# Optimization experiments

Hardware: AMD Instinct MI355X
Metric: run time of the kernel (lower is better)

Reference implementation:

```python
import jax, jax.numpy as jnp
import numpy as np

B, S, D_MODEL, D_K, D_V = 4, 2048, 1024, 64, 64


def setup_inputs() -> dict:
    key = jax.random.key(0)
    ks = jax.random.split(key, 6)
    Q = jax.random.normal(ks[0], (B, S, D_MODEL), dtype=jnp.float32)
    K = jax.random.normal(ks[1], (B, S, D_MODEL), dtype=jnp.float32)
    V = jax.random.normal(ks[2], (B, S, D_MODEL), dtype=jnp.float32)
    # Linear weights stored as [in, out] so projection is x @ W
    scale = 1.0 / np.sqrt(D_MODEL)
    WQ = jax.random.normal(ks[3], (D_MODEL, D_K), dtype=jnp.float32) * scale
    WK = jax.random.normal(ks[4], (D_MODEL, D_K), dtype=jnp.float32) * scale
    WV = jax.random.normal(ks[5], (D_MODEL, D_V), dtype=jnp.float32) * scale
    # causal mask: 1 = attend, 0 = masked (torch masked_fill(mask == 0, -inf))
    mask = jnp.tril(jnp.ones((S, S), dtype=jnp.int32))
    return {"Q": Q, "K": K, "V": V, "WQ": WQ, "WK": WK, "WV": WV, "mask": mask}


def reference(Q, K, V, WQ, WK, WV, mask):
    d_k = WQ.shape[-1]
    q = jnp.einsum("bsd,dk->bsk", Q, WQ)   # [B,S,d_k]
    k = jnp.einsum("bsd,dk->bsk", K, WK)   # [B,S,d_k]
    v = jnp.einsum("bsd,dv->bsv", V, WV)   # [B,S,d_v]
    scores = jnp.einsum("bqk,bsk->bqs", q, k) / jnp.sqrt(jnp.float32(d_k))
    scores = jnp.where(mask == 0, -jnp.inf, scores)  # broadcast [S,S] over batch
    attn = jax.nn.softmax(scores, axis=-1)
    H = jnp.einsum("bqs,bsv->bqv", attn, v)  # [B,S,d_v]
    return H
```

## Files before the change

### kernel.cpp

```cpp
#include <hip/hip_runtime.h>

typedef unsigned int u32;
typedef unsigned short u16;
using bf16x8 = __attribute__((ext_vector_type(8))) short;
using f32x4  = __attribute__((ext_vector_type(4))) float;

#define MFMA16 __builtin_amdgcn_mfma_f32_16x16x32_bf16

#define QH  (0u)
#define QL  (1u<<20)
#define KHO (2u<<20)
#define KLO (3u<<20)
#define VHO (4u<<20)
#define VLO (5u<<20)
#define VTH (6u<<20)
#define VTL (7u<<20)
#define WTH (8u<<20)
#define WTL (WTH + 3u*64*1024*2)
#define OPOFF (9u<<20)
#define PMOFF (OPOFF + 576u*4096*4)
#define PLOFF (PMOFF + 576u*64*4)

__device__ __forceinline__ u16 f2bf(float x) {
    u32 u = __float_as_uint(x);
    return (u16)((u + 0x7FFFu + ((u >> 16) & 1u)) >> 16);
}
__device__ __forceinline__ float bf2f(u16 h) {
    return __uint_as_float(((u32)h) << 16);
}

__device__ __forceinline__ int swz(int row, int c) {
    return c ^ ((row ^ (row >> 3)) & 7);
}
__device__ __forceinline__ bf16x8 ldsf(const char* t, int row, int c) {
    return *reinterpret_cast<const bf16x8*>(t + row * 128 + swz(row, c) * 16);
}
__device__ __forceinline__ void ldst(char* t, int row, int c, bf16x8 v) {
    *reinterpret_cast<bf16x8*>(t + row * 128 + swz(row, c) * 16) = v;
}

__device__ __forceinline__ void stage_bf16(char* tile, const u16* g, int ldu, int t) {
    const int row = t >> 2, cg = t & 3;
    const char* gp = reinterpret_cast<const char*>(g + (size_t)row * ldu + cg * 16);
    bf16x8 a = *reinterpret_cast<const bf16x8*>(gp);
    bf16x8 b = *reinterpret_cast<const bf16x8*>(gp + 16);
    ldst(tile, row, cg * 2, a);
    ldst(tile, row, cg * 2 + 1, b);
}

__device__ __forceinline__ void stage_split(char* th, char* tl, const float* g, int ld, int t) {
    const int row = t >> 2, cg = t & 3;
    const float* gp = g + (size_t)row * ld + cg * 16;
    #pragma unroll
    for (int c = 0; c < 2; ++c) {
        bf16x8 h, l;
        #pragma unroll
        for (int j = 0; j < 8; ++j) {
            float x = gp[c * 8 + j];
            u16 hb = f2bf(x);
            u16 lb = f2bf(x - bf2f(hb));
            h[j] = (short)hb; l[j] = (short)lb;
        }
        ldst(th, row, cg * 2 + c, h);
        ldst(tl, row, cg * 2 + c, l);
    }
}

__global__ __launch_bounds__(256) void wsplit_kernel(const float* __restrict__ WQ,
                                                     const float* __restrict__ WK,
                                                     const float* __restrict__ WV,
                                                     char* __restrict__ ws) {
    const int p = blockIdx.y, kt = blockIdx.x;
    const float* W = (p == 0) ? WQ : (p == 1) ? WK : WV;
    __shared__ float lds[64 * 68];
    const int t = threadIdx.x, row = t >> 2, cg = t & 3;
    const float* gp = W + ((size_t)kt * 64 + row) * 64 + cg * 16;
    #pragma unroll
    for (int j = 0; j < 16; ++j) lds[row * 68 + cg * 16 + j] = gp[j];
    __syncthreads();
    const int n = row, d0 = cg * 16;
    u32 wh[8], wl[8];
    #pragma unroll
    for (int j = 0; j < 8; ++j) {
        float x0 = lds[(d0 + 2 * j) * 68 + n];
        float x1 = lds[(d0 + 2 * j + 1) * 68 + n];
        u16 h0 = f2bf(x0), h1 = f2bf(x1);
        u16 l0 = f2bf(x0 - bf2f(h0)), l1 = f2bf(x1 - bf2f(h1));
        wh[j] = (u32)h0 | ((u32)h1 << 16);
        wl[j] = (u32)l0 | ((u32)l1 << 16);
    }
    u16* oh = (u16*)(ws + WTH) + (size_t)p * 64 * 1024 + (size_t)n * 1024 + kt * 64 + d0;
    u16* ol = (u16*)(ws + WTL) + (size_t)p * 64 * 1024 + (size_t)n * 1024 + kt * 64 + d0;
    uint4 a = {wh[0], wh[1], wh[2], wh[3]}, b = {wh[4], wh[5], wh[6], wh[7]};
    uint4 c = {wl[0], wl[1], wl[2], wl[3]}, d = {wl[4], wl[5], wl[6], wl[7]};
    *reinterpret_cast<uint4*>(oh) = a; *reinterpret_cast<uint4*>(oh + 8) = b;
    *reinterpret_cast<uint4*>(ol) = c; *reinterpret_cast<uint4*>(ol + 8) = d;
}

__global__ __launch_bounds__(256) void proj_kernel(const float* __restrict__ Q,
                                                   const float* __restrict__ K,
                                                   const float* __restrict__ V,
                                                   char* __restrict__ ws) {
    const int p = blockIdx.y;
    const float* X = (p == 0) ? Q : (p == 1) ? K : V;
    const u16* wth = (const u16*)(ws + WTH) + (size_t)p * 64 * 1024;
    const u16* wtl = (const u16*)(ws + WTL) + (size_t)p * 64 * 1024;
    u16* oh = (u16*)(ws + ((p == 0) ? QH : (p == 1) ? KHO : VHO));
    u16* ol = (u16*)(ws + ((p == 0) ? QL : (p == 1) ? KLO : VLO));
    const int rt = blockIdx.x;
    __shared__ char xh[8192], xl[8192], bh_[8192], bl_[8192];
    const int t = threadIdx.x, lane = t & 63, w = t >> 6;
    f32x4 acc[4];
    #pragma unroll
    for (int nt = 0; nt < 4; ++nt) acc[nt] = (f32x4){0.f, 0.f, 0.f, 0.f};
    for (int kc = 0; kc < 1024; kc += 64) {
        __syncthreads();
        stage_split(xh, xl, X + (size_t)rt * 64 * 1024 + kc, 1024, t);
        stage_bf16(bh_, wth + kc, 1024, t);
        stage_bf16(bl_, wtl + kc, 1024, t);
        __syncthreads();
        #pragma unroll
        for (int s = 0; s < 2; ++s) {
            bf16x8 ah = ldsf(xh, w * 16 + (lane & 15), s * 4 + (lane >> 4));
            bf16x8 al = ldsf(xl, w * 16 + (lane & 15), s * 4 + (lane >> 4));
            #pragma unroll
            for (int nt = 0; nt < 4; ++nt) {
                bf16x8 bh = ldsf(bh_, nt * 16 + (lane & 15), s * 4 + (lane >> 4));
                bf16x8 bl = ldsf(bl_, nt * 16 + (lane & 15), s * 4 + (lane >> 4));
                acc[nt] = MFMA16(ah, bh, acc[nt], 0, 0, 0);
                acc[nt] = MFMA16(ah, bl, acc[nt], 0, 0, 0);
                acc[nt] = MFMA16(al, bh, acc[nt], 0, 0, 0);
            }
        }
    }
    const float qs = (p == 0) ? 0.125f : 1.0f;
    #pragma unroll
    for (int nt = 0; nt < 4; ++nt)
        #pragma unroll
        for (int r = 0; r < 4; ++r) {
            float v = acc[nt][r] * qs;
            u16 hb = f2bf(v);
            u16 lb = f2bf(v - bf2f(hb));
            size_t idx = ((size_t)rt * 64 + w * 16 + (lane >> 4) * 4 + r) * 64 + nt * 16 + (lane & 15);
            oh[idx] = hb; ol[idx] = lb;
        }
}

__global__ __launch_bounds__(256) void vt_kernel(char* __restrict__ ws) {
    const int st = blockIdx.x, b = blockIdx.y;
    __shared__ u16 lh[64 * 72], ll[64 * 72];
    const int t = threadIdx.x, row = t >> 2, cg = t & 3;
    const u16* vh = (const u16*)(ws + VHO) + ((size_t)b * 2048 + st * 64 + row) * 64 + cg * 16;
    const u16* vl = (const u16*)(ws + VLO) + ((size_t)b * 2048 + st * 64 + row) * 64 + cg * 16;
    *reinterpret_cast<uint4*>(&lh[row * 72 + cg * 16]) = *reinterpret_cast<const uint4*>(vh);
    *reinterpret_cast<uint4*>(&lh[row * 72 + cg * 16 + 8]) = *reinterpret_cast<const uint4*>(vh + 8);
    *reinterpret_cast<uint4*>(&ll[row * 72 + cg * 16]) = *reinterpret_cast<const uint4*>(vl);
    *reinterpret_cast<uint4*>(&ll[row * 72 + cg * 16 + 8]) = *reinterpret_cast<const uint4*>(vl + 8);
    __syncthreads();
    const int d = row, s0 = cg * 16;
    u32 wh[8], wl[8];
    #pragma unroll
    for (int j = 0; j < 8; ++j) {
        wh[j] = (u32)lh[(s0 + 2 * j) * 72 + d] | ((u32)lh[(s0 + 2 * j + 1) * 72 + d] << 16);
        wl[j] = (u32)ll[(s0 + 2 * j) * 72 + d] | ((u32)ll[(s0 + 2 * j + 1) * 72 + d] << 16);
    }
    u16* th = (u16*)(ws + VTH) + ((size_t)b * 64 + d) * 2048 + st * 64 + s0;
    u16* tl = (u16*)(ws + VTL) + ((size_t)b * 64 + d) * 2048 + st * 64 + s0;
    uint4 a = {wh[0], wh[1], wh[2], wh[3]}, bb = {wh[4], wh[5], wh[6], wh[7]};
    uint4 c = {wl[0], wl[1], wl[2], wl[3]}, dd = {wl[4], wl[5], wl[6], wl[7]};
    *reinterpret_cast<uint4*>(th) = a; *reinterpret_cast<uint4*>(th + 8) = bb;
    *reinterpret_cast<uint4*>(tl) = c; *reinterpret_cast<uint4*>(tl + 8) = dd;
}

__device__ __forceinline__ int slot_base(int qt) {
    const int q4 = qt >> 2, r = qt & 3;
    return qt + 2 * q4 * (q4 - 1) + r * q4;
}

__global__ __launch_bounds__(256) void attn_kernel(char* __restrict__ ws) {
    const int chunk = blockIdx.x;
    const int qt = 31 - blockIdx.y;
    const int b = blockIdx.z;
    const int Li = qt + 1, kt0 = chunk * 4;
    if (kt0 >= Li) return;
    const int kt1 = (kt0 + 4 < Li) ? kt0 + 4 : Li;
    __shared__ char kh[8192], kl[8192], vh[8192], vl[8192], ph[8192], pl[8192];
    const int t = threadIdx.x, lane = t & 63, w = t >> 6;
    const u16* qhg = (const u16*)(ws + QH);
    const u16* qlg = (const u16*)(ws + QL);
    const size_t qrow = (size_t)b * 2048 + qt * 64 + w * 16 + (lane & 15);
    bf16x8 qfh[2], qfl[2];
    #pragma unroll
    for (int s = 0; s < 2; ++s) {
        qfh[s] = *reinterpret_cast<const bf16x8*>(qhg + qrow * 64 + s * 32 + (lane >> 4) * 8);
        qfl[s] = *reinterpret_cast<const bf16x8*>(qlg + qrow * 64 + s * 32 + (lane >> 4) * 8);
    }
    const u16* kgh = (const u16*)(ws + KHO) + (size_t)b * 2048 * 64;
    const u16* kgl = (const u16*)(ws + KLO) + (size_t)b * 2048 * 64;
    const u16* vgh = (const u16*)(ws + VTH) + (size_t)b * 64 * 2048;
    const u16* vgl = (const u16*)(ws + VTL) + (size_t)b * 64 * 2048;
    f32x4 o[4];
    #pragma unroll
    for (int nt = 0; nt < 4; ++nt) o[nt] = (f32x4){0.f, 0.f, 0.f, 0.f};
    float mrow[4], lrow[4];
    #pragma unroll
    for (int r = 0; r < 4; ++r) { mrow[r] = -1e30f; lrow[r] = 0.f; }
    for (int kt = kt0; kt < kt1; ++kt) {
        __syncthreads();
        stage_bf16(kh, kgh + (size_t)kt * 64 * 64, 64, t);
        stage_bf16(kl, kgl + (size_t)kt * 64 * 64, 64, t);
        stage_bf16(vh, vgh + kt * 64, 2048, t);
        stage_bf16(vl, vgl + kt * 64, 2048, t);
        __syncthreads();
        f32x4 sacc[4];
        #pragma unroll
        for (int nt = 0; nt < 4; ++nt) sacc[nt] = (f32x4){0.f, 0.f, 0.f, 0.f};
        #pragma unroll
        for (int s = 0; s < 2; ++s) {
            #pragma unroll
            for (int nt = 0; nt < 4; ++nt) {
                bf16x8 bh = ldsf(kh, nt * 16 + (lane & 15), s * 4 + (lane >> 4));
                bf16x8 bl = ldsf(kl, nt * 16 + (lane & 15), s * 4 + (lane >> 4));
                sacc[nt] = MFMA16(qfh[s], bh, sacc[nt], 0, 0, 0);
                sacc[nt] = MFMA16(qfh[s], bl, sacc[nt], 0, 0, 0);
                sacc[nt] = MFMA16(qfl[s], bh, sacc[nt], 0, 0, 0);
            }
        }
        if (kt == qt) {
            #pragma unroll
            for (int nt = 0; nt < 4; ++nt)
                #pragma unroll
                for (int r = 0; r < 4; ++r)
                    if (nt * 16 + (lane & 15) > w * 16 + (lane >> 4) * 4 + r)
                        sacc[nt][r] = -1e30f;
        }
        float pcur[4][4], scv[4];
        #pragma unroll
        for (int r = 0; r < 4; ++r) {
            float mx = fmaxf(fmaxf(sacc[0][r], sacc[1][r]), fmaxf(sacc[2][r], sacc[3][r]));
            #pragma unroll
            for (int off = 1; off < 16; off <<= 1) mx = fmaxf(mx, __shfl_xor(mx, off));
            const float nm = fmaxf(mrow[r], mx);
            scv[r] = __expf(mrow[r] - nm);
            mrow[r] = nm;
            float rs = 0.f;
            #pragma unroll
            for (int nt = 0; nt < 4; ++nt) {
                float pv = __expf(sacc[nt][r] - nm);
                pcur[nt][r] = pv; rs += pv;
            }
            #pragma unroll
            for (int off = 1; off < 16; off <<= 1) rs += __shfl_xor(rs, off);
            lrow[r] = lrow[r] * scv[r] + rs;
        }
        f32x4 scq = {scv[0], scv[1], scv[2], scv[3]};
        #pragma unroll
        for (int nt = 0; nt < 4; ++nt) o[nt] *= scq;
        #pragma unroll
        for (int nt = 0; nt < 4; ++nt)
            #pragma unroll
            for (int r = 0; r < 4; ++r) {
                const int row = w * 16 + (lane >> 4) * 4 + r;
                const int key = nt * 16 + (lane & 15);
                u16 hb = f2bf(pcur[nt][r]);
                u16 lb = f2bf(pcur[nt][r] - bf2f(hb));
                const int byt = row * 128 + swz(row, key >> 3) * 16 + (key & 7) * 2;
                *reinterpret_cast<u16*>(ph + byt) = hb;
                *reinterpret_cast<u16*>(pl + byt) = lb;
            }
        #pragma unroll
        for (int s = 0; s < 2; ++s) {
            bf16x8 pah = ldsf(ph, w * 16 + (lane & 15), s * 4 + (lane >> 4));
            bf16x8 pal = ldsf(pl, w * 16 + (lane & 15), s * 4 + (lane >> 4));
            #pragma unroll
            for (int nt = 0; nt < 4; ++nt) {
                bf16x8 vbh = ldsf(vh, nt * 16 + (lane & 15), s * 4 + (lane >> 4));
                bf16x8 vbl = ldsf(vl, nt * 16 + (lane & 15), s * 4 + (lane >> 4));
                o[nt] = MFMA16(pah, vbh, o[nt], 0, 0, 0);
                o[nt] = MFMA16(pah, vbl, o[nt], 0, 0, 0);
                o[nt] = MFMA16(pal, vbh, o[nt], 0, 0, 0);
            }
        }
    }
    const int slot = b * 144 + slot_base(qt) + chunk;
    float* Op = (float*)(ws + OPOFF) + (size_t)slot * 4096;
    #pragma unroll
    for (int nt = 0; nt < 4; ++nt)
        #pragma unroll
        for (int r = 0; r < 4; ++r)
            Op[(size_t)(w * 16 + (lane >> 4) * 4 + r) * 64 + nt * 16 + (lane & 15)] = o[nt][r];
    if ((lane & 15) == 0) {
        float* Pm = (float*)(ws + PMOFF);
        float* Pl = (float*)(ws + PLOFF);
        #pragma unroll
        for (int r = 0; r < 4; ++r) {
            Pm[(size_t)slot * 64 + w * 16 + (lane >> 4) * 4 + r] = mrow[r];
            Pl[(size_t)slot * 64 + w * 16 + (lane >> 4) * 4 + r] = lrow[r];
        }
    }
}

__global__ __launch_bounds__(256) void merge_kernel(const char* __restrict__ ws,
                                                    float* __restrict__ out) {
    const int qt = blockIdx.x, b = blockIdx.y;
    const int Ci = (qt >> 2) + 1;
    const int slot0 = b * 144 + slot_base(qt);
    const float* Op = (const float*)(ws + OPOFF);
    const float* Pm = (const float*)(ws + PMOFF);
    const float* Pl = (const float*)(ws + PLOFF);
    const int t = threadIdx.x, d = t & 63, rg = t >> 6;
    for (int rv = 0; rv < 16; ++rv) {
        const int row = rg + rv * 4;
        float M = -1e30f;
        for (int c = 0; c < Ci; ++c) M = fmaxf(M, Pm[(size_t)(slot0 + c) * 64 + row]);
        float den = 0.f, acc = 0.f;
        for (int c = 0; c < Ci; ++c) {
            const float wv = __expf(Pm[(size_t)(slot0 + c) * 64 + row] - M);
            den += wv * Pl[(size_t)(slot0 + c) * 64 + row];
            acc += wv * Op[(size_t)(slot0 + c) * 4096 + (size_t)row * 64 + d];
        }
        out[(size_t)((b * 32 + qt) * 64 + row) * 64 + d] = acc / den;
    }
}

extern "C" void kernel_launch(void* const* d_in, const int* in_sizes, int n_in,
                              void* d_out, int out_size, void* d_ws, size_t ws_size,
                              hipStream_t stream) {
    (void)in_sizes; (void)n_in; (void)out_size; (void)ws_size;
    const float* Q  = (const float*)d_in[0];
    const float* K  = (const float*)d_in[1];
    const float* V  = (const float*)d_in[2];
    const float* WQ = (const float*)d_in[3];
    const float* WK = (const float*)d_in[4];
    const float* WV = (const float*)d_in[5];
    char* ws   = (char*)d_ws;
    float* out = (float*)d_out;

    wsplit_kernel<<<dim3(16, 3), dim3(256), 0, stream>>>(WQ, WK, WV, ws);
    proj_kernel<<<dim3(128, 3), dim3(256), 0, stream>>>(Q, K, V, ws);
    vt_kernel<<<dim3(32, 4), dim3(256), 0, stream>>>(ws);
    attn_kernel<<<dim3(8, 32, 4), dim3(256), 0, stream>>>(ws);
    merge_kernel<<<dim3(32, 4), dim3(256), 0, stream>>>(ws, out);
}
```

Baseline: 237.8 us.

## Register-prefetch next tiles in projection and attention, widen merge grid

The projection and attention kernels now load the next K-chunk or key tile from global memory into registers while the current tile is being computed. This overlaps global-load latency with MFMA work in place of the previous synchronous staging. X loads are vectorized as float4. The merge kernel now launches one block per group of 4 rows instead of looping over 64 rows, which gives many more blocks for parallelism. The cost is higher register pressure from the double-buffered register sets.

```diff
diff --git a/kernel.cpp b/kernel.cpp
--- a/kernel.cpp
+++ b/kernel.cpp
@@ -39,30 +39,13 @@
     *reinterpret_cast<bf16x8*>(t + row * 128 + swz(row, c) * 16) = v;
 }
 
-__device__ __forceinline__ void stage_bf16(char* tile, const u16* g, int ldu, int t) {
-    const int row = t >> 2, cg = t & 3;
-    const char* gp = reinterpret_cast<const char*>(g + (size_t)row * ldu + cg * 16);
-    bf16x8 a = *reinterpret_cast<const bf16x8*>(gp);
-    bf16x8 b = *reinterpret_cast<const bf16x8*>(gp + 16);
-    ldst(tile, row, cg * 2, a);
-    ldst(tile, row, cg * 2 + 1, b);
-}
-
-__device__ __forceinline__ void stage_split(char* th, char* tl, const float* g, int ld, int t) {
-    const int row = t >> 2, cg = t & 3;
-    const float* gp = g + (size_t)row * ld + cg * 16;
-    #pragma unroll
-    for (int c = 0; c < 2; ++c) {
-        bf16x8 h, l;
-        #pragma unroll
-        for (int j = 0; j < 8; ++j) {
-            float x = gp[c * 8 + j];
-            u16 hb = f2bf(x);
-            u16 lb = f2bf(x - bf2f(hb));
-            h[j] = (short)hb; l[j] = (short)lb;
-        }
-        ldst(th, row, cg * 2 + c, h);
-        ldst(tl, row, cg * 2 + c, l);
+__device__ __forceinline__ void split8(float4 v0, float4 v1, bf16x8& h, bf16x8& l) {
+    float e[8] = {v0.x, v0.y, v0.z, v0.w, v1.x, v1.y, v1.z, v1.w};
+    #pragma unroll
+    for (int j = 0; j < 8; ++j) {
+        u16 hb = f2bf(e[j]);
+        h[j] = (short)hb;
+        l[j] = (short)f2bf(e[j] - bf2f(hb));
     }
 }
 
@@ -110,14 +93,38 @@
     const int rt = blockIdx.x;
     __shared__ char xh[8192], xl[8192], bh_[8192], bl_[8192];
     const int t = threadIdx.x, lane = t & 63, w = t >> 6;
+    const int rs = t >> 2, cs = t & 3;
+
+    auto ldrow = [&](int kc, float4* xr, bf16x8* wr) {
+        const float* gp = X + (size_t)rt * 64 * 1024 + (size_t)rs * 1024 + kc + cs * 16;
+        xr[0] = *reinterpret_cast<const float4*>(gp);
+        xr[1] = *reinterpret_cast<const float4*>(gp + 4);
+        xr[2] = *reinterpret_cast<const float4*>(gp + 8);
+        xr[3] = *reinterpret_cast<const float4*>(gp + 12);
+        const u16* ph_ = wth + (size_t)rs * 1024 + kc + cs * 16;
+        const u16* pl_ = wtl + (size_t)rs * 1024 + kc + cs * 16;
+        wr[0] = *reinterpret_cast<const bf16x8*>(ph_);
+        wr[1] = *reinterpret_cast<const bf16x8*>(ph_ + 8);
+        wr[2] = *reinterpret_cast<const bf16x8*>(pl_);
+        wr[3] = *reinterpret_cast<const bf16x8*>(pl_ + 8);
+    };
+
     f32x4 acc[4];
     #pragma unroll
     for (int nt = 0; nt < 4; ++nt) acc[nt] = (f32x4){0.f, 0.f, 0.f, 0.f};
+    float4 xc[4], xn[4];
+    bf16x8 wc[4], wn[4];
+    ldrow(0, xc, wc);
     for (int kc = 0; kc < 1024; kc += 64) {
         __syncthreads();
-        stage_split(xh, xl, X + (size_t)rt * 64 * 1024 + kc, 1024, t);
-        stage_bf16(bh_, wth + kc, 1024, t);
-        stage_bf16(bl_, wtl + kc, 1024, t);
+        bf16x8 h0, l0, h1, l1;
+        split8(xc[0], xc[1], h0, l0);
+        split8(xc[2], xc[3], h1, l1);
+        ldst(xh, rs, cs * 2, h0);     ldst(xl, rs, cs * 2, l0);
+        ldst(xh, rs, cs * 2 + 1, h1); ldst(xl, rs, cs * 2 + 1, l1);
+        ldst(bh_, rs, cs * 2, wc[0]); ldst(bh_, rs, cs * 2 + 1, wc[1]);
+        ldst(bl_, rs, cs * 2, wc[2]); ldst(bl_, rs, cs * 2 + 1, wc[3]);
+        if (kc + 64 < 1024) ldrow(kc + 64, xn, wn);
         __syncthreads();
         #pragma unroll
         for (int s = 0; s < 2; ++s) {
@@ -132,6 +139,8 @@
                 acc[nt] = MFMA16(al, bh, acc[nt], 0, 0, 0);
             }
         }
+        #pragma unroll
+        for (int i = 0; i < 4; ++i) { xc[i] = xn[i]; wc[i] = wn[i]; }
     }
     const float qs = (p == 0) ? 0.125f : 1.0f;
     #pragma unroll
@@ -186,6 +195,7 @@
     const int kt1 = (kt0 + 4 < Li) ? kt0 + 4 : Li;
     __shared__ char kh[8192], kl[8192], vh[8192], vl[8192], ph[8192], pl[8192];
     const int t = threadIdx.x, lane = t & 63, w = t >> 6;
+    const int rs = t >> 2, cs = t & 3;
     const u16* qhg = (const u16*)(ws + QH);
     const u16* qlg = (const u16*)(ws + QL);
     const size_t qrow = (size_t)b * 2048 + qt * 64 + w * 16 + (lane & 15);
@@ -199,18 +209,41 @@
     const u16* kgl = (const u16*)(ws + KLO) + (size_t)b * 2048 * 64;
     const u16* vgh = (const u16*)(ws + VTH) + (size_t)b * 64 * 2048;
     const u16* vgl = (const u16*)(ws + VTL) + (size_t)b * 64 * 2048;
+
+    auto ldreg = [&](int kt, bf16x8* r) {
+        const u16* pk_h = kgh + (size_t)kt * 4096 + (size_t)rs * 64 + cs * 16;
+        const u16* pk_l = kgl + (size_t)kt * 4096 + (size_t)rs * 64 + cs * 16;
+        const u16* pv_h = vgh + (size_t)rs * 2048 + kt * 64 + cs * 16;
+        const u16* pv_l = vgl + (size_t)rs * 2048 + kt * 64 + cs * 16;
+        r[0] = *reinterpret_cast<const bf16x8*>(pk_h);
+        r[1] = *reinterpret_cast<const bf16x8*>(pk_h + 8);
+        r[2] = *reinterpret_cast<const bf16x8*>(pk_l);
+        r[3] = *reinterpret_cast<const bf16x8*>(pk_l + 8);
+        r[4] = *reinterpret_cast<const bf16x8*>(pv_h);
+        r[5] = *reinterpret_cast<const bf16x8*>(pv_h + 8);
+        r[6] = *reinterpret_cast<const bf16x8*>(pv_l);
+        r[7] = *reinterpret_cast<const bf16x8*>(pv_l + 8);
+    };
+    auto stlds = [&](bf16x8* r) {
+        ldst(kh, rs, cs * 2, r[0]); ldst(kh, rs, cs * 2 + 1, r[1]);
+        ldst(kl, rs, cs * 2, r[2]); ldst(kl, rs, cs * 2 + 1, r[3]);
+        ldst(vh, rs, cs * 2, r[4]); ldst(vh, rs, cs * 2 + 1, r[5]);
+        ldst(vl, rs, cs * 2, r[6]); ldst(vl, rs, cs * 2 + 1, r[7]);
+    };
+
     f32x4 o[4];
     #pragma unroll
     for (int nt = 0; nt < 4; ++nt) o[nt] = (f32x4){0.f, 0.f, 0.f, 0.f};
     float mrow[4], lrow[4];
     #pragma unroll
     for (int r = 0; r < 4; ++r) { mrow[r] = -1e30f; lrow[r] = 0.f; }
+
+    bf16x8 rc[8], rn[8];
+    ldreg(kt0, rc);
     for (int kt = kt0; kt < kt1; ++kt) {
         __syncthreads();
-        stage_bf16(kh, kgh + (size_t)kt * 64 * 64, 64, t);
-        stage_bf16(kl, kgl + (size_t)kt * 64 * 64, 64, t);
-        stage_bf16(vh, vgh + kt * 64, 2048, t);
-        stage_bf16(vl, vgl + kt * 64, 2048, t);
+        stlds(rc);
+        if (kt + 1 < kt1) ldreg(kt + 1, rn);
         __syncthreads();
         f32x4 sacc[4];
         #pragma unroll
@@ -243,15 +276,15 @@
             const float nm = fmaxf(mrow[r], mx);
             scv[r] = __expf(mrow[r] - nm);
             mrow[r] = nm;
-            float rs = 0.f;
+            float rs_ = 0.f;
             #pragma unroll
             for (int nt = 0; nt < 4; ++nt) {
                 float pv = __expf(sacc[nt][r] - nm);
-                pcur[nt][r] = pv; rs += pv;
-            }
-            #pragma unroll
-            for (int off = 1; off < 16; off <<= 1) rs += __shfl_xor(rs, off);
-            lrow[r] = lrow[r] * scv[r] + rs;
+                pcur[nt][r] = pv; rs_ += pv;
+            }
+            #pragma unroll
+            for (int off = 1; off < 16; off <<= 1) rs_ += __shfl_xor(rs_, off);
+            lrow[r] = lrow[r] * scv[r] + rs_;
         }
         f32x4 scq = {scv[0], scv[1], scv[2], scv[3]};
         #pragma unroll
@@ -281,6 +314,8 @@
                 o[nt] = MFMA16(pal, vbh, o[nt], 0, 0, 0);
             }
         }
+        #pragma unroll
+        for (int i = 0; i < 8; ++i) rc[i] = rn[i];
     }
     const int slot = b * 144 + slot_base(qt) + chunk;
     float* Op = (float*)(ws + OPOFF) + (size_t)slot * 4096;
@@ -302,25 +337,23 @@
 
 __global__ __launch_bounds__(256) void merge_kernel(const char* __restrict__ ws,
                                                     float* __restrict__ out) {
-    const int qt = blockIdx.x, b = blockIdx.y;
+    const int qt = blockIdx.x >> 4, rb = blockIdx.x & 15, b = blockIdx.y;
+    const int t = threadIdx.x, d = t & 63, rloc = t >> 6;
+    const int row = rb * 4 + rloc;
     const int Ci = (qt >> 2) + 1;
     const int slot0 = b * 144 + slot_base(qt);
     const float* Op = (const float*)(ws + OPOFF);
     const float* Pm = (const float*)(ws + PMOFF);
     const float* Pl = (const float*)(ws + PLOFF);
-    const int t = threadIdx.x, d = t & 63, rg = t >> 6;
-    for (int rv = 0; rv < 16; ++rv) {
-        const int row = rg + rv * 4;
-        float M = -1e30f;
-        for (int c = 0; c < Ci; ++c) M = fmaxf(M, Pm[(size_t)(slot0 + c) * 64 + row]);
-        float den = 0.f, acc = 0.f;
-        for (int c = 0; c < Ci; ++c) {
-            const float wv = __expf(Pm[(size_t)(slot0 + c) * 64 + row] - M);
-            den += wv * Pl[(size_t)(slot0 + c) * 64 + row];
-            acc += wv * Op[(size_t)(slot0 + c) * 4096 + (size_t)row * 64 + d];
-        }
-        out[(size_t)((b * 32 + qt) * 64 + row) * 64 + d] = acc / den;
-    }
+    float M = -1e30f;
+    for (int c = 0; c < Ci; ++c) M = fmaxf(M, Pm[(size_t)(slot0 + c) * 64 + row]);
+    float den = 0.f, acc = 0.f;
+    for (int c = 0; c < Ci; ++c) {
+        const float wv = __expf(Pm[(size_t)(slot0 + c) * 64 + row] - M);
+        den += wv * Pl[(size_t)(slot0 + c) * 64 + row];
+        acc += wv * Op[(size_t)(slot0 + c) * 4096 + (size_t)row * 64 + d];
+    }
+    out[(size_t)((b * 32 + qt) * 64 + row) * 64 + d] = acc / den;
 }
 
 extern "C" void kernel_launch(void* const* d_in, const int* in_sizes, int n_in,
@@ -340,5 +373,5 @@
     proj_kernel<<<dim3(128, 3), dim3(256), 0, stream>>>(Q, K, V, ws);
     vt_kernel<<<dim3(32, 4), dim3(256), 0, stream>>>(ws);
     attn_kernel<<<dim3(8, 32, 4), dim3(256), 0, stream>>>(ws);
-    merge_kernel<<<dim3(32, 4), dim3(256), 0, stream>>>(ws, out);
-}
+    merge_kernel<<<dim3(512, 4), dim3(256), 0, stream>>>(ws, out);
+}
```

Result: faster. 191.4 us (-19.5%).
